# Performance work log

Measured on AMD Instinct MI355X. Metric: run time of the kernel, lower is better.

## Reference

```python
import jax, jax.numpy as jnp
import numpy as np

FEATURE_LEN = 64
DIM_ATOM = 256
DIM_GRAPH = 256
NUM_NEI = 32
B = 2048          # reactions / graphs in batch
ATOMS = 30        # atoms per molecule graph
N = B * ATOMS     # total nodes
E = 4 * N         # total edges
NMOL = 100000     # knowledge-graph molecule table size
S = 2             # molecules per reaction side (len(id_list))


def setup_inputs() -> dict:
    key = jax.random.key(0)
    ks = jax.random.split(key, 16)
    xavier = lambda k, shape: (jax.random.normal(k, shape, jnp.float32)
                               * np.sqrt(2.0 / (shape[0] + shape[-1])))
    return {
        "node_feat": jax.random.randint(ks[0], (N, 4), 0, FEATURE_LEN, jnp.int32),
        "edge_src": jax.random.randint(ks[1], (E,), 0, N, jnp.int32),
        "edge_dst": jax.random.randint(ks[2], (E,), 0, N, jnp.int32),
        "graph_ids": jnp.repeat(jnp.arange(B, dtype=jnp.int32), ATOMS),
        "id_list": jax.random.randint(ks[3], (S, B), 0, NMOL, jnp.int32),
        "id_list_target": jax.random.randint(ks[4], (S, B), 0, NMOL, jnp.int32),
        "all_mfea": (jax.random.uniform(ks[5], (NMOL, 40)) < 0.3).astype(jnp.float32),
        "neighbor_matrix": jax.random.randint(ks[6], (NMOL, NUM_NEI), 0, NMOL, jnp.int32),
        "W0": xavier(ks[7], (FEATURE_LEN, DIM_ATOM)),
        "b0": jnp.zeros((DIM_ATOM,), jnp.float32),
        "W1": xavier(ks[8], (DIM_ATOM, DIM_ATOM)),
        "b1": jnp.zeros((DIM_ATOM,), jnp.float32),
        "fea_emb": xavier(ks[9], (40, DIM_GRAPH)),
        "att_w": xavier(ks[10], (DIM_GRAPH, 1)),
        "att_b": jnp.zeros((1,), jnp.float32),
        "crosscl_w": xavier(ks[11], (DIM_GRAPH, DIM_ATOM)),
        "crosscl_b": jnp.zeros((DIM_ATOM,), jnp.float32),
    }


def reference(node_feat, edge_src, edge_dst, graph_ids, id_list, id_list_target,
              all_mfea, neighbor_matrix,
              W0, b0, W1, b1, fea_emb, att_w, att_b, crosscl_w, crosscl_b):
    n = node_feat.shape[0]
    # --- atom-level GCN (DGL GraphConv, norm='both') ---
    h = jax.nn.one_hot(node_feat, FEATURE_LEN, dtype=jnp.float32).sum(axis=1)  # [N, F]
    ones_e = jnp.ones((edge_src.shape[0],), jnp.float32)
    deg_out = jnp.clip(jax.ops.segment_sum(ones_e, edge_src, n), 1.0)
    deg_in = jnp.clip(jax.ops.segment_sum(ones_e, edge_dst, n), 1.0)
    norm_src = deg_out[:, None] ** -0.5
    norm_dst = deg_in[:, None] ** -0.5

    def gcn(x, W, b, act):
        m = (x * norm_src)[edge_src]                        # gather along edges
        agg = jax.ops.segment_sum(m, edge_dst, n)           # scatter-add
        z = (agg * norm_dst) @ W + b
        return act(z)

    h = gcn(h, W0, b0, jax.nn.relu)
    h = gcn(h, W1, b1, lambda z: z)
    # factor computed via python float() in torch -> detached constant
    factor = np.sqrt(DIM_ATOM).astype(np.float32) / jax.lax.stop_gradient(
        jnp.mean(jnp.linalg.norm(h, axis=1)))
    h = h * factor
    mol_atom_embedding = jax.ops.segment_sum(h, graph_ids, B)  # SumPooling [B, D]

    # --- reaction-level KG aggregation ---
    src_emb = jnp.einsum('sbf,fg->sbg', all_mfea[id_list], fea_emb)         # [S,B,G]
    tgt_emb = jnp.einsum('sbf,fg->sbg', all_mfea[id_list_target], fea_emb)  # [S,B,G]
    source_re = src_emb.mean(axis=0)   # 1/len * sum
    target_re = tgt_emb.mean(axis=0)

    item_emb = src_emb                                       # [S,B,G]
    nei_idx = neighbor_matrix[id_list]                       # [S,B,K]
    nei_emb = jnp.einsum('sbkf,fg->sbkg', all_mfea[nei_idx], fea_emb)  # [S,B,K,G]

    target_embedding = source_re + target_re                 # [B,G]
    score_nei = item_emb[:, :, None, :] * nei_emb * target_embedding[None, :, None, :]
    logits = score_nei @ att_w + att_b                       # [S,B,K,1]
    score_att = jax.nn.softmax(logits, axis=2)
    nei_agg = jnp.sum(score_att * nei_emb, axis=2)           # [S,B,G]

    mol_reaction_embedding = (item_emb + nei_agg).mean(axis=0)  # [B,G]
    mol_x_embedding = mol_reaction_embedding @ crosscl_w + crosscl_b
    mol_embedding = jnp.concatenate([mol_atom_embedding, mol_reaction_embedding], axis=1)
    return mol_embedding, mol_atom_embedding, mol_x_embedding
```

## Files before the change

### kernel.cpp

```cpp
#include <hip/hip_runtime.h>
#include <math.h>

#define N_NODES 61440
#define N_EDGES 245760
#define BATCH   2048
#define ATOMS   30
#define F_LEN   64
#define DIM     256
#define NUM_NEI 32
#define MF      40
#define ECAP    512
#define CH      32
#define NBG     (N_NODES / 32)

typedef __attribute__((ext_vector_type(8))) short s8v;
typedef __attribute__((ext_vector_type(4))) float f4v;
typedef __attribute__((address_space(3))) unsigned lds_u32;
typedef const __attribute__((address_space(1))) unsigned glb_u32;

__device__ __forceinline__ unsigned short f2bf(float x) {
    union { float f; unsigned u; } c; c.f = x;
    unsigned r = (c.u + 0x7FFFu + ((c.u >> 16) & 1u)) >> 16;
    return (unsigned short)r;
}
__device__ __forceinline__ float bf2f(unsigned short u) {
    union { unsigned u; float f; } c; c.u = ((unsigned)u) << 16;
    return c.f;
}
__device__ __forceinline__ float u2f(unsigned u) {
    union { unsigned u; float f; } c; c.u = u;
    return c.f;
}

__global__ __launch_bounds__(256) void k_deg_prepw(
    const int* __restrict__ esrc, const int* __restrict__ edst,
    int* deg_out, int* deg_in,
    const float* __restrict__ W0, const float* __restrict__ W1,
    unsigned short* __restrict__ w0bt, unsigned short* __restrict__ w1bt) {
    __shared__ float tile[64][65];
    int bi = blockIdx.x;
    int t = threadIdx.x;
    if (bi < 960) {
        int e = bi * 256 + t;
        atomicAdd(&deg_out[esrc[e]], 1);
        atomicAdd(&deg_in[edst[e]], 1);
        return;
    }
    int b2 = bi - 960;
    int c = t & 63, rq = t >> 6;
    if (b2 < 16) {
        int tr = b2 >> 2, tc = b2 & 3;
#pragma unroll 4
        for (int pass = 0; pass < 16; pass++) {
            int r = rq + 4 * pass;
            tile[r][c] = W1[(size_t)(tr * 64 + r) * 256 + tc * 64 + c];
        }
        __syncthreads();
#pragma unroll 4
        for (int pass = 0; pass < 16; pass++) {
            int nr = rq + 4 * pass;
            w1bt[(size_t)(tc * 64 + nr) * 256 + tr * 64 + c] = f2bf(tile[c][nr]);
        }
    } else {
        int tb = b2 - 16;
#pragma unroll 4
        for (int pass = 0; pass < 16; pass++) {
            int r = rq + 4 * pass;
            tile[r][c] = W0[(size_t)r * 256 + tb * 64 + c];
        }
        __syncthreads();
#pragma unroll 4
        for (int pass = 0; pass < 16; pass++) {
            int nr = rq + 4 * pass;
            w0bt[(size_t)(tb * 64 + nr) * 64 + c] = f2bf(tile[c][nr]);
        }
    }
}

__global__ void k_alloc(const int* __restrict__ deg_in, int* row_start, int* cursor,
                        int* counter) {
    int t = threadIdx.x;
    int n = blockIdx.x * 256 + t;
    int lane = t & 63;
    int d = deg_in[n];
    int p = d;
#pragma unroll
    for (int o = 1; o < 64; o <<= 1) { int v = __shfl_up(p, o, 64); if (lane >= o) p += v; }
    int base = 0;
    if (lane == 63) base = atomicAdd(counter, p);
    base = __shfl(base, 63, 64);
    int v = base + p - d;
    row_start[n] = v;
    cursor[n] = v;
}

__global__ void k_csr_fill(const int* __restrict__ esrc, const int* __restrict__ edst,
                           int* cursor, int* csr_src) {
    int e = blockIdx.x * 256 + threadIdx.x;
    if (e < N_EDGES) {
        int p = atomicAdd(&cursor[edst[e]], 1);
        csr_src[p] = esrc[e];
    }
}

__global__ __launch_bounds__(256) void k_gcn0(
    const int* __restrict__ nf, const int* __restrict__ row_start,
    const int* __restrict__ csr_src, const int* __restrict__ deg_in,
    const int* __restrict__ deg_out, const unsigned short* __restrict__ w0bt,
    const float* __restrict__ b0, unsigned short* __restrict__ h1b) {
    __shared__ float la0[32 * 68];
    __shared__ int4  enf[ECAP];
    __shared__ float ens[ECAP];
    __shared__ int   rs[33];
    __shared__ float lnd[32], lns[32];
    __shared__ float b0c[256];
    int n0 = blockIdx.x * 32;
    int t = threadIdx.x;
    if (t < 32) rs[t] = row_start[n0 + t];
    if (t == 0) rs[32] = row_start[n0 + 31] + deg_in[n0 + 31];
    if (t < 32) {
        lnd[t] = rsqrtf((float)max(deg_in[n0 + t], 1));
        lns[t] = rsqrtf((float)max(deg_out[n0 + t], 1));
    }
    b0c[t] = b0[t];
    for (int i = t; i < 32 * 68; i += 256) la0[i] = 0.f;
    __syncthreads();
    int beg0 = rs[0];
    int tot = rs[32] - beg0; if (tot > ECAP) tot = ECAP;
    for (int e = t; e < tot; e += 256) {
        int s = csr_src[beg0 + e];
        enf[e] = ((const int4*)nf)[s];
        ens[e] = rsqrtf((float)max(deg_out[s], 1));
    }
    __syncthreads();
    if (t < 128) {
        int row = t >> 2, fi = t & 3;
        int lo = rs[row] - beg0, hi = rs[row + 1] - beg0;
        if (hi > tot) hi = tot;
        for (int e = lo; e < hi; e++) {
            int4 f = enf[e];
            int fv = (fi == 0) ? f.x : (fi == 1) ? f.y : (fi == 2) ? f.z : f.w;
            atomicAdd(&la0[row * 68 + fv], ens[e]);
        }
    }
    __syncthreads();
    int lane = t & 63, wv = t >> 6;
    int ln = lane & 15, lg = lane >> 4;
    f4v acc[2][4];
#pragma unroll
    for (int mi = 0; mi < 2; mi++)
#pragma unroll
        for (int ni = 0; ni < 4; ni++) acc[mi][ni] = (f4v)0.f;
#pragma unroll
    for (int kst = 0; kst < 2; kst++) {
        s8v afr[2];
#pragma unroll
        for (int mi = 0; mi < 2; mi++) {
            const float* p = &la0[(mi * 16 + ln) * 68 + kst * 32 + lg * 8];
            f4v lo = *(const f4v*)p;
            f4v hi = *(const f4v*)(p + 4);
            s8v a;
#pragma unroll
            for (int j = 0; j < 4; j++) { a[j] = (short)f2bf(lo[j]); a[4 + j] = (short)f2bf(hi[j]); }
            afr[mi] = a;
        }
#pragma unroll
        for (int ni = 0; ni < 4; ni++) {
            int n = wv * 64 + ni * 16 + ln;
            s8v b = *(const s8v*)&w0bt[(size_t)n * 64 + kst * 32 + lg * 8];
            acc[0][ni] = __builtin_amdgcn_mfma_f32_16x16x32_bf16(afr[0], b, acc[0][ni], 0, 0, 0);
            acc[1][ni] = __builtin_amdgcn_mfma_f32_16x16x32_bf16(afr[1], b, acc[1][ni], 0, 0, 0);
        }
    }
#pragma unroll
    for (int mi = 0; mi < 2; mi++)
#pragma unroll
        for (int ni = 0; ni < 4; ni++) {
            int n = wv * 64 + ni * 16 + ln;
            float bb = b0c[n];
#pragma unroll
            for (int r = 0; r < 4; r++) {
                int m = mi * 16 + lg * 4 + r;
                float z = acc[mi][ni][r] * lnd[m] + bb;
                z = fmaxf(z, 0.f) * lns[m];
                h1b[(size_t)(n0 + m) * 256 + n] = f2bf(z);
            }
        }
}

__global__ __launch_bounds__(256, 4) void k_gcn1rxn(
    const unsigned short* __restrict__ h1b, const int* __restrict__ row_start,
    const int* __restrict__ csr_src, const int* __restrict__ deg_in,
    const unsigned short* __restrict__ w1bt, const float* __restrict__ b1,
    unsigned short* __restrict__ h2b, float* __restrict__ partial,
    const int* __restrict__ id_list, const int* __restrict__ id_list_t,
    const int* __restrict__ neimat, const float* __restrict__ mfea,
    const float* __restrict__ fea_emb, const float* __restrict__ att_w,
    const float* __restrict__ att_b, float* __restrict__ mre_out,
    float* __restrict__ out) {
    __shared__ __attribute__((aligned(16))) char smem[36992];
    int bid = blockIdx.x;
    int t = threadIdx.x;
    int lane = t & 63, wv = t >> 6;
    bool isg; int sub;
    if (bid < 2 * NBG) { isg = !(bid & 1); sub = bid >> 1; }
    else { isg = false; sub = NBG + (bid - 2 * NBG); }

    if (isg) {
        unsigned short* stage = (unsigned short*)smem;
        int*   ecache = (int*)(smem + 32768);
        int*   rs     = (int*)(smem + 34816);
        float* lnd    = (float*)(smem + 34960);
        float* b1c    = (float*)(smem + 35088);
        float* nsq    = (float*)(smem + 36112);
        unsigned short* lab = stage;
        int n0 = sub * 32;
        if (t < 32) rs[t] = row_start[n0 + t];
        if (t == 0) rs[32] = row_start[n0 + 31] + deg_in[n0 + 31];
        if (t < 32) {
            lnd[t] = rsqrtf((float)max(deg_in[n0 + t], 1));
            nsq[t] = 0.f;
        }
        b1c[t] = b1[t];
        __syncthreads();
        int beg0 = rs[0];
        int tot = rs[32] - beg0; if (tot > ECAP) tot = ECAP;
        for (int e = t; e < tot; e += 256) ecache[e] = csr_src[beg0 + e];
        __syncthreads();

        int gr = t >> 5;
        int gc = (t & 31) * 8;
        int lo[4], hi[4];
#pragma unroll
        for (int r = 0; r < 4; r++) {
            int i = gr + r * 8;
            lo[r] = rs[i] - beg0;
            int h = rs[i + 1] - beg0; if (h > tot) h = tot;
            hi[r] = h;
        }
        float a[4][8];
#pragma unroll
        for (int r = 0; r < 4; r++)
#pragma unroll
            for (int j = 0; j < 8; j++) a[r][j] = 0.f;

        int lhalf = lane >> 5;
        int colo = (lane & 31) * 8;
        int nc = (tot + CH - 1) >> 5;
#define ISSUE(c)                                                                   \
        {                                                                          \
            int base_ = (c) << 5;                                                  \
            unsigned short* sb_ = stage + ((c) & 1) * (CH * 256);                  \
            _Pragma("unroll")                                                      \
            for (int pp = 0; pp < 4; ++pp) {                                       \
                int p_ = wv + pp * 4;                                              \
                int e_ = base_ + 2 * p_ + lhalf;                                   \
                int sv_ = ecache[min(e_, tot - 1)];                                \
                __builtin_amdgcn_global_load_lds(                                  \
                    (glb_u32*)(h1b + (size_t)sv_ * 256 + colo),                    \
                    (lds_u32*)(sb_ + 2 * p_ * 256), 16, 0, 0);                     \
            }                                                                      \
        }
        if (nc > 0) ISSUE(0);
        for (int c = 0; c < nc; ++c) {
            if (c + 1 < nc) {
                ISSUE(c + 1);
                asm volatile("s_waitcnt vmcnt(4)" ::: "memory");
            } else {
                asm volatile("s_waitcnt vmcnt(0)" ::: "memory");
            }
            __builtin_amdgcn_sched_barrier(0);
            __builtin_amdgcn_s_barrier();
            int c0 = c << 5;
            int nch = min(CH, tot - c0);
            const unsigned short* sb = stage + (c & 1) * (CH * 256);
#pragma unroll
            for (int r = 0; r < 4; r++) {
                int es = max(lo[r] - c0, 0);
                int ee = min(hi[r] - c0, nch);
                for (int e = es; e < ee; e++) {
                    s8v v = *(const s8v*)&sb[e * 256 + gc];
#pragma unroll
                    for (int j = 0; j < 8; j++) a[r][j] += bf2f((unsigned short)v[j]);
                }
            }
            __builtin_amdgcn_s_barrier();
        }
#undef ISSUE
#pragma unroll
        for (int r = 0; r < 4; r++) {
            int i = gr + r * 8;
            s8v ov;
#pragma unroll
            for (int j = 0; j < 8; j++) ov[j] = (short)f2bf(a[r][j]);
            *(s8v*)&lab[i * 264 + gc] = ov;
        }
        __syncthreads();
        int ln = lane & 15, lg = lane >> 4;
        f4v acc[2][4];
#pragma unroll
        for (int mi = 0; mi < 2; mi++)
#pragma unroll
            for (int ni = 0; ni < 4; ni++) acc[mi][ni] = (f4v)0.f;
#pragma unroll 2
        for (int kst = 0; kst < 8; kst++) {
            s8v afr[2];
#pragma unroll
            for (int mi = 0; mi < 2; mi++)
                afr[mi] = *(const s8v*)&lab[(mi * 16 + ln) * 264 + kst * 32 + lg * 8];
#pragma unroll
            for (int ni = 0; ni < 4; ni++) {
                int n = wv * 64 + ni * 16 + ln;
                s8v b = *(const s8v*)&w1bt[(size_t)n * 256 + kst * 32 + lg * 8];
                acc[0][ni] = __builtin_amdgcn_mfma_f32_16x16x32_bf16(afr[0], b, acc[0][ni], 0, 0, 0);
                acc[1][ni] = __builtin_amdgcn_mfma_f32_16x16x32_bf16(afr[1], b, acc[1][ni], 0, 0, 0);
            }
        }
        float sm[2][4];
#pragma unroll
        for (int mi = 0; mi < 2; mi++)
#pragma unroll
            for (int r = 0; r < 4; r++) sm[mi][r] = 0.f;
#pragma unroll
        for (int mi = 0; mi < 2; mi++)
#pragma unroll
            for (int ni = 0; ni < 4; ni++) {
                int n = wv * 64 + ni * 16 + ln;
                float bb = b1c[n];
#pragma unroll
                for (int r = 0; r < 4; r++) {
                    int m = mi * 16 + lg * 4 + r;
                    float z = acc[mi][ni][r] * lnd[m] + bb;
                    h2b[(size_t)(n0 + m) * 256 + n] = f2bf(z);
                    sm[mi][r] += z * z;
                }
            }
#pragma unroll
        for (int mi = 0; mi < 2; mi++)
#pragma unroll
            for (int r = 0; r < 4; r++) {
                float v = sm[mi][r];
                v += __shfl_xor(v, 1);
                v += __shfl_xor(v, 2);
                v += __shfl_xor(v, 4);
                v += __shfl_xor(v, 8);
                if (ln == 0) atomicAdd(&nsq[mi * 16 + lg * 4 + r], v);
            }
        __syncthreads();
        if (t < 32) atomicAdd(&partial[(n0 + t) & 1023], sqrtf(nsq[t]));
    } else {
        float* com   = (float*)smem;
        float* mitem = (float*)(smem + 160);
        float* u     = (float*)(smem + 320);
        float* nm    = (float*)(smem + 1344);
        float* vv    = (float*)(smem + 6464);
        float* aw    = (float*)(smem + 6624);
        int b = sub;
        if (t < MF) {
            int i0 = id_list[b], i1 = id_list[BATCH + b];
            int j0 = id_list_t[b], j1 = id_list_t[BATCH + b];
            com[t] = 0.5f * (mfea[(size_t)i0 * MF + t] + mfea[(size_t)i1 * MF + t])
                   + 0.5f * (mfea[(size_t)j0 * MF + t] + mfea[(size_t)j1 * MF + t]);
        }
        __syncthreads();
        float tg = 0.f;
        for (int f = 0; f < MF; f++) tg += com[f] * fea_emb[f * DIM + t];
        float awt = att_w[t];
        float msum = 0.f;
        for (int s = 0; s < 2; s++) {
            int id = id_list[s * BATCH + b];
            __syncthreads();
            if (t < MF) mitem[t] = mfea[(size_t)id * MF + t];
            for (int i = t; i < NUM_NEI * 10; i += 256) {
                int k = i / 10, q = i - k * 10;
                int nid = neimat[(size_t)id * NUM_NEI + k];
                *(float4*)&nm[k * MF + q * 4] = *(const float4*)&mfea[(size_t)nid * MF + q * 4];
            }
            __syncthreads();
            float item = 0.f;
            for (int f = 0; f < MF; f++) item += mitem[f] * fea_emb[f * DIM + t];
            u[t] = item * tg * awt;
            __syncthreads();
            for (int i = 0; i < 5; i++) {
                int f = wv + 8 * i;
                float p = 0.f;
#pragma unroll
                for (int j = 0; j < 4; j++) p += u[lane + 64 * j] * fea_emb[f * DIM + lane + 64 * j];
#pragma unroll
                for (int off = 32; off; off >>= 1) p += __shfl_down(p, off, 64);
                if (lane == 0) vv[f] = p;
            }
            __syncthreads();
            if (wv == 0) {
                float lg2 = -1e30f;
                if (lane < NUM_NEI) {
                    lg2 = att_b[0];
                    for (int f = 0; f < MF; f++) lg2 += nm[lane * MF + f] * vv[f];
                }
                float m = lg2;
#pragma unroll
                for (int off = 16; off; off >>= 1) m = fmaxf(m, __shfl_xor(m, off, 32));
                float e = (lane < NUM_NEI) ? __expf(lg2 - m) : 0.f;
                float ssum = e;
#pragma unroll
                for (int off = 16; off; off >>= 1) ssum += __shfl_xor(ssum, off, 32);
                if (lane < NUM_NEI) aw[lane] = e / ssum;
            }
            __syncthreads();
            if (t < MF) {
                float w = 0.f;
                for (int k = 0; k < NUM_NEI; k++) w += aw[k] * nm[k * MF + t];
                vv[t] = w;
            }
            __syncthreads();
            float na = 0.f;
            for (int f = 0; f < MF; f++) na += vv[f] * fea_emb[f * DIM + t];
            msum += item + na;
        }
        float m = 0.5f * msum;
        out[(size_t)b * 512 + DIM + t] = m;
        mre_out[(size_t)b * DIM + t] = m;
    }
}

__global__ __launch_bounds__(256) void k_fin(
    const unsigned short* __restrict__ h2b, const float* __restrict__ partial,
    const float* __restrict__ mre, const float* __restrict__ cw,
    const float* __restrict__ cb, float* __restrict__ out) {
    __shared__ float red[256];
    __shared__ float lm[8 * DIM];
    int t = threadIdx.x;
    int b0 = blockIdx.x * 8;
    float s = partial[t] + partial[t + 256] + partial[t + 512] + partial[t + 768];
    red[t] = s;
    __syncthreads();
    for (int o = 128; o; o >>= 1) {
        if (t < o) red[t] += red[t + o];
        __syncthreads();
    }
    float fac = 16.0f * (float)N_NODES / red[0];
#pragma unroll 2
    for (int i = 0; i < 8; i++) {
        float pv = 0.f;
        for (int a = 0; a < ATOMS; a++)
            pv += bf2f(h2b[(size_t)((b0 + i) * ATOMS + a) * DIM + t]);
        pv *= fac;
        out[(size_t)(b0 + i) * 512 + t] = pv;
        out[(size_t)BATCH * 512 + (size_t)(b0 + i) * DIM + t] = pv;
    }
    for (int i = t; i < 8 * DIM / 4; i += 256)
        ((float4*)lm)[i] = ((const float4*)(mre + (size_t)b0 * DIM))[i];
    __syncthreads();
    float acc[8];
    float bb = cb[t];
#pragma unroll
    for (int i = 0; i < 8; i++) acc[i] = bb;
    for (int uu = 0; uu < DIM; uu++) {
        float w = cw[(size_t)uu * DIM + t];
#pragma unroll
        for (int i = 0; i < 8; i++) acc[i] += lm[i * DIM + uu] * w;
    }
#pragma unroll
    for (int i = 0; i < 8; i++)
        out[(size_t)BATCH * 768 + (size_t)(b0 + i) * DIM + t] = acc[i];
}

extern "C" void kernel_launch(void* const* d_in, const int* in_sizes, int n_in,
                              void* d_out, int out_size, void* d_ws, size_t ws_size,
                              hipStream_t stream) {
    const int*   node_feat = (const int*)d_in[0];
    const int*   edge_src  = (const int*)d_in[1];
    const int*   edge_dst  = (const int*)d_in[2];
    const int*   id_list   = (const int*)d_in[4];
    const int*   id_list_t = (const int*)d_in[5];
    const float* all_mfea  = (const float*)d_in[6];
    const int*   neimat    = (const int*)d_in[7];
    const float* W0        = (const float*)d_in[8];
    const float* b0        = (const float*)d_in[9];
    const float* W1        = (const float*)d_in[10];
    const float* b1        = (const float*)d_in[11];
    const float* fea_emb   = (const float*)d_in[12];
    const float* att_w     = (const float*)d_in[13];
    const float* att_b     = (const float*)d_in[14];
    const float* crosscl_w = (const float*)d_in[15];
    const float* crosscl_b = (const float*)d_in[16];
    float* out = (float*)d_out;

    char* ws = (char*)d_ws;
    char* zbase = ws;
    int*   deg_out   = (int*)ws;            ws += (size_t)N_NODES * 4;
    int*   deg_in    = (int*)ws;            ws += (size_t)N_NODES * 4;
    float* partial   = (float*)ws;          ws += 1024 * 4;
    int*   counter   = (int*)(ws + 8);      ws += 256;
    size_t zbytes = (size_t)(ws - zbase);
    int*   row_start = (int*)ws;            ws += (size_t)N_NODES * 4;
    int*   cursor    = (int*)ws;            ws += (size_t)N_NODES * 4;
    int*   csr_srcb  = (int*)ws;            ws += (size_t)N_EDGES * 4;
    unsigned short* w0bt = (unsigned short*)ws; ws += (size_t)256 * 64 * 2;
    unsigned short* w1bt = (unsigned short*)ws; ws += (size_t)256 * 256 * 2;
    unsigned short* h1b  = (unsigned short*)ws; ws += (size_t)N_NODES * DIM * 2;
    unsigned short* h2b  = (unsigned short*)ws; ws += (size_t)N_NODES * DIM * 2;
    float* mre       = (float*)ws;          ws += (size_t)BATCH * DIM * 4;

    hipMemsetAsync(zbase, 0, zbytes, stream);

    k_deg_prepw<<<980, 256, 0, stream>>>(edge_src, edge_dst, deg_out, deg_in,
                                         W0, W1, w0bt, w1bt);
    k_alloc<<<N_NODES / 256, 256, 0, stream>>>(deg_in, row_start, cursor, counter);
    k_csr_fill<<<(N_EDGES + 255) / 256, 256, 0, stream>>>(edge_src, edge_dst, cursor, csr_srcb);
    k_gcn0<<<N_NODES / 32, 256, 0, stream>>>(node_feat, row_start, csr_srcb, deg_in,
                                             deg_out, w0bt, b0, h1b);
    k_gcn1rxn<<<2 * NBG + (BATCH - NBG), 256, 0, stream>>>(
        h1b, row_start, csr_srcb, deg_in, w1bt, b1, h2b, partial,
        id_list, id_list_t, neimat, all_mfea, fea_emb, att_w, att_b, mre, out);
    k_fin<<<BATCH / 8, 256, 0, stream>>>(h2b, partial, mre, crosscl_w, crosscl_b, out);
}
```

Measured before the change: 198.2 us.

## Split fused GCN-layer-1 and reaction kernel into two separate launches

Splits the combined kernel, which interleaved GCN layer-1 aggregation/GEMM blocks with reaction-level KG attention blocks, into two kernels launched back to back on the same stream. Each kernel now has its own static shared-memory footprint, so the light reaction kernel no longer reserves the large staging buffer and may reach higher occupancy. The cost is an extra launch and the loss of overlap between the memory-bound gather work and the latency-bound reaction work.

Result: faster. 186.1 us (median of 3 runs) (-6.1%).

```diff
diff --git a/kernel.cpp b/kernel.cpp
--- a/kernel.cpp
+++ b/kernel.cpp
@@ -11,7 +11,6 @@
 #define MF      40
 #define ECAP    512
 #define CH      32
-#define NBG     (N_NODES / 32)
 
 typedef __attribute__((ext_vector_type(8))) short s8v;
 typedef __attribute__((ext_vector_type(4))) float f4v;
@@ -25,10 +24,6 @@
 }
 __device__ __forceinline__ float bf2f(unsigned short u) {
     union { unsigned u; float f; } c; c.u = ((unsigned)u) << 16;
-    return c.f;
-}
-__device__ __forceinline__ float u2f(unsigned u) {
-    union { unsigned u; float f; } c; c.u = u;
     return c.f;
 }
 
@@ -188,239 +183,235 @@
         }
 }
 
-__global__ __launch_bounds__(256, 4) void k_gcn1rxn(
+__global__ __launch_bounds__(256, 4) void k_gcn1(
     const unsigned short* __restrict__ h1b, const int* __restrict__ row_start,
     const int* __restrict__ csr_src, const int* __restrict__ deg_in,
     const unsigned short* __restrict__ w1bt, const float* __restrict__ b1,
-    unsigned short* __restrict__ h2b, float* __restrict__ partial,
+    unsigned short* __restrict__ h2b, float* __restrict__ partial) {
+    __shared__ unsigned short stage[2 * CH * 256];
+    __shared__ int   ecache[ECAP];
+    __shared__ int   rs[33];
+    __shared__ float lnd[32];
+    __shared__ float b1c[256];
+    __shared__ float nsq[32];
+    unsigned short* lab = stage;
+    int n0 = blockIdx.x * 32;
+    int t = threadIdx.x;
+    int lane = t & 63, wv = t >> 6;
+    if (t < 32) rs[t] = row_start[n0 + t];
+    if (t == 0) rs[32] = row_start[n0 + 31] + deg_in[n0 + 31];
+    if (t < 32) {
+        lnd[t] = rsqrtf((float)max(deg_in[n0 + t], 1));
+        nsq[t] = 0.f;
+    }
+    b1c[t] = b1[t];
+    __syncthreads();
+    int beg0 = rs[0];
+    int tot = rs[32] - beg0; if (tot > ECAP) tot = ECAP;
+    for (int e = t; e < tot; e += 256) ecache[e] = csr_src[beg0 + e];
+    __syncthreads();
+
+    int gr = t >> 5;
+    int gc = (t & 31) * 8;
+    int lo[4], hi[4];
+#pragma unroll
+    for (int r = 0; r < 4; r++) {
+        int i = gr + r * 8;
+        lo[r] = rs[i] - beg0;
+        int h = rs[i + 1] - beg0; if (h > tot) h = tot;
+        hi[r] = h;
+    }
+    float a[4][8];
+#pragma unroll
+    for (int r = 0; r < 4; r++)
+#pragma unroll
+        for (int j = 0; j < 8; j++) a[r][j] = 0.f;
+
+    int lhalf = lane >> 5;
+    int colo = (lane & 31) * 8;
+    int nc = (tot + CH - 1) >> 5;
+#define ISSUE(c)                                                                   \
+    {                                                                              \
+        int base_ = (c) << 5;                                                      \
+        unsigned short* sb_ = stage + ((c) & 1) * (CH * 256);                      \
+        _Pragma("unroll")                                                          \
+        for (int pp = 0; pp < 4; ++pp) {                                           \
+            int p_ = wv + pp * 4;                                                  \
+            int e_ = base_ + 2 * p_ + lhalf;                                       \
+            int sv_ = ecache[min(e_, tot - 1)];                                    \
+            __builtin_amdgcn_global_load_lds(                                      \
+                (glb_u32*)(h1b + (size_t)sv_ * 256 + colo),                        \
+                (lds_u32*)(sb_ + 2 * p_ * 256), 16, 0, 0);                         \
+        }                                                                          \
+    }
+    if (nc > 0) ISSUE(0);
+    for (int c = 0; c < nc; ++c) {
+        if (c + 1 < nc) {
+            ISSUE(c + 1);
+            asm volatile("s_waitcnt vmcnt(4)" ::: "memory");
+        } else {
+            asm volatile("s_waitcnt vmcnt(0)" ::: "memory");
+        }
+        __builtin_amdgcn_sched_barrier(0);
+        __builtin_amdgcn_s_barrier();
+        int c0 = c << 5;
+        int nch = min(CH, tot - c0);
+        const unsigned short* sb = stage + (c & 1) * (CH * 256);
+#pragma unroll
+        for (int r = 0; r < 4; r++) {
+            int es = max(lo[r] - c0, 0);
+            int ee = min(hi[r] - c0, nch);
+            for (int e = es; e < ee; e++) {
+                s8v v = *(const s8v*)&sb[e * 256 + gc];
+#pragma unroll
+                for (int j = 0; j < 8; j++) a[r][j] += bf2f((unsigned short)v[j]);
+            }
+        }
+        __builtin_amdgcn_s_barrier();
+    }
+#undef ISSUE
+#pragma unroll
+    for (int r = 0; r < 4; r++) {
+        int i = gr + r * 8;
+        s8v ov;
+#pragma unroll
+        for (int j = 0; j < 8; j++) ov[j] = (short)f2bf(a[r][j]);
+        *(s8v*)&lab[i * 264 + gc] = ov;
+    }
+    __syncthreads();
+    int ln = lane & 15, lg = lane >> 4;
+    f4v acc[2][4];
+#pragma unroll
+    for (int mi = 0; mi < 2; mi++)
+#pragma unroll
+        for (int ni = 0; ni < 4; ni++) acc[mi][ni] = (f4v)0.f;
+#pragma unroll 2
+    for (int kst = 0; kst < 8; kst++) {
+        s8v afr[2];
+#pragma unroll
+        for (int mi = 0; mi < 2; mi++)
+            afr[mi] = *(const s8v*)&lab[(mi * 16 + ln) * 264 + kst * 32 + lg * 8];
+#pragma unroll
+        for (int ni = 0; ni < 4; ni++) {
+            int n = wv * 64 + ni * 16 + ln;
+            s8v b = *(const s8v*)&w1bt[(size_t)n * 256 + kst * 32 + lg * 8];
+            acc[0][ni] = __builtin_amdgcn_mfma_f32_16x16x32_bf16(afr[0], b, acc[0][ni], 0, 0, 0);
+            acc[1][ni] = __builtin_amdgcn_mfma_f32_16x16x32_bf16(afr[1], b, acc[1][ni], 0, 0, 0);
+        }
+    }
+    float sm[2][4];
+#pragma unroll
+    for (int mi = 0; mi < 2; mi++)
+#pragma unroll
+        for (int r = 0; r < 4; r++) sm[mi][r] = 0.f;
+#pragma unroll
+    for (int mi = 0; mi < 2; mi++)
+#pragma unroll
+        for (int ni = 0; ni < 4; ni++) {
+            int n = wv * 64 + ni * 16 + ln;
+            float bb = b1c[n];
+#pragma unroll
+            for (int r = 0; r < 4; r++) {
+                int m = mi * 16 + lg * 4 + r;
+                float z = acc[mi][ni][r] * lnd[m] + bb;
+                h2b[(size_t)(n0 + m) * 256 + n] = f2bf(z);
+                sm[mi][r] += z * z;
+            }
+        }
+#pragma unroll
+    for (int mi = 0; mi < 2; mi++)
+#pragma unroll
+        for (int r = 0; r < 4; r++) {
+            float v = sm[mi][r];
+            v += __shfl_xor(v, 1);
+            v += __shfl_xor(v, 2);
+            v += __shfl_xor(v, 4);
+            v += __shfl_xor(v, 8);
+            if (ln == 0) atomicAdd(&nsq[mi * 16 + lg * 4 + r], v);
+        }
+    __syncthreads();
+    if (t < 32) atomicAdd(&partial[(n0 + t) & 1023], sqrtf(nsq[t]));
+}
+
+__global__ __launch_bounds__(256) void k_rxn(
     const int* __restrict__ id_list, const int* __restrict__ id_list_t,
     const int* __restrict__ neimat, const float* __restrict__ mfea,
     const float* __restrict__ fea_emb, const float* __restrict__ att_w,
     const float* __restrict__ att_b, float* __restrict__ mre_out,
     float* __restrict__ out) {
-    __shared__ __attribute__((aligned(16))) char smem[36992];
-    int bid = blockIdx.x;
+    __shared__ float com[MF];
+    __shared__ float mitem[MF];
+    __shared__ float u[DIM];
+    __shared__ float nm[NUM_NEI * MF];
+    __shared__ float vv[MF];
+    __shared__ float aw[NUM_NEI];
+    int b = blockIdx.x;
     int t = threadIdx.x;
-    int lane = t & 63, wv = t >> 6;
-    bool isg; int sub;
-    if (bid < 2 * NBG) { isg = !(bid & 1); sub = bid >> 1; }
-    else { isg = false; sub = NBG + (bid - 2 * NBG); }
-
-    if (isg) {
-        unsigned short* stage = (unsigned short*)smem;
-        int*   ecache = (int*)(smem + 32768);
-        int*   rs     = (int*)(smem + 34816);
-        float* lnd    = (float*)(smem + 34960);
-        float* b1c    = (float*)(smem + 35088);
-        float* nsq    = (float*)(smem + 36112);
-        unsigned short* lab = stage;
-        int n0 = sub * 32;
-        if (t < 32) rs[t] = row_start[n0 + t];
-        if (t == 0) rs[32] = row_start[n0 + 31] + deg_in[n0 + 31];
-        if (t < 32) {
-            lnd[t] = rsqrtf((float)max(deg_in[n0 + t], 1));
-            nsq[t] = 0.f;
-        }
-        b1c[t] = b1[t];
-        __syncthreads();
-        int beg0 = rs[0];
-        int tot = rs[32] - beg0; if (tot > ECAP) tot = ECAP;
-        for (int e = t; e < tot; e += 256) ecache[e] = csr_src[beg0 + e];
-        __syncthreads();
-
-        int gr = t >> 5;
-        int gc = (t & 31) * 8;
-        int lo[4], hi[4];
-#pragma unroll
-        for (int r = 0; r < 4; r++) {
-            int i = gr + r * 8;
-            lo[r] = rs[i] - beg0;
-            int h = rs[i + 1] - beg0; if (h > tot) h = tot;
-            hi[r] = h;
-        }
-        float a[4][8];
-#pragma unroll
-        for (int r = 0; r < 4; r++)
-#pragma unroll
-            for (int j = 0; j < 8; j++) a[r][j] = 0.f;
-
-        int lhalf = lane >> 5;
-        int colo = (lane & 31) * 8;
-        int nc = (tot + CH - 1) >> 5;
-#define ISSUE(c)                                                                   \
-        {                                                                          \
-            int base_ = (c) << 5;                                                  \
-            unsigned short* sb_ = stage + ((c) & 1) * (CH * 256);                  \
-            _Pragma("unroll")                                                      \
-            for (int pp = 0; pp < 4; ++pp) {                                       \
-                int p_ = wv + pp * 4;                                              \
-                int e_ = base_ + 2 * p_ + lhalf;                                   \
-                int sv_ = ecache[min(e_, tot - 1)];                                \
-                __builtin_amdgcn_global_load_lds(                                  \
-                    (glb_u32*)(h1b + (size_t)sv_ * 256 + colo),                    \
-                    (lds_u32*)(sb_ + 2 * p_ * 256), 16, 0, 0);                     \
-            }                                                                      \
-        }
-        if (nc > 0) ISSUE(0);
-        for (int c = 0; c < nc; ++c) {
-            if (c + 1 < nc) {
-                ISSUE(c + 1);
-                asm volatile("s_waitcnt vmcnt(4)" ::: "memory");
-            } else {
-                asm volatile("s_waitcnt vmcnt(0)" ::: "memory");
+    int wv = t >> 6, lane = t & 63;
+    if (t < MF) {
+        int i0 = id_list[b], i1 = id_list[BATCH + b];
+        int j0 = id_list_t[b], j1 = id_list_t[BATCH + b];
+        com[t] = 0.5f * (mfea[(size_t)i0 * MF + t] + mfea[(size_t)i1 * MF + t])
+               + 0.5f * (mfea[(size_t)j0 * MF + t] + mfea[(size_t)j1 * MF + t]);
+    }
+    __syncthreads();
+    float tg = 0.f;
+    for (int f = 0; f < MF; f++) tg += com[f] * fea_emb[f * DIM + t];
+    float awt = att_w[t];
+    float msum = 0.f;
+    for (int s = 0; s < 2; s++) {
+        int id = id_list[s * BATCH + b];
+        __syncthreads();
+        if (t < MF) mitem[t] = mfea[(size_t)id * MF + t];
+        for (int i = t; i < NUM_NEI * 10; i += 256) {
+            int k = i / 10, q = i - k * 10;
+            int nid = neimat[(size_t)id * NUM_NEI + k];
+            *(float4*)&nm[k * MF + q * 4] = *(const float4*)&mfea[(size_t)nid * MF + q * 4];
+        }
+        __syncthreads();
+        float item = 0.f;
+        for (int f = 0; f < MF; f++) item += mitem[f] * fea_emb[f * DIM + t];
+        u[t] = item * tg * awt;
+        __syncthreads();
+        for (int i = 0; i < 5; i++) {
+            int f = wv + 8 * i;
+            float p = 0.f;
+#pragma unroll
+            for (int j = 0; j < 4; j++) p += u[lane + 64 * j] * fea_emb[f * DIM + lane + 64 * j];
+#pragma unroll
+            for (int off = 32; off; off >>= 1) p += __shfl_down(p, off, 64);
+            if (lane == 0) vv[f] = p;
+        }
+        __syncthreads();
+        if (wv == 0) {
+            float lg2 = -1e30f;
+            if (lane < NUM_NEI) {
+                lg2 = att_b[0];
+                for (int f = 0; f < MF; f++) lg2 += nm[lane * MF + f] * vv[f];
             }
-            __builtin_amdgcn_sched_barrier(0);
-            __builtin_amdgcn_s_barrier();
-            int c0 = c << 5;
-            int nch = min(CH, tot - c0);
-            const unsigned short* sb = stage + (c & 1) * (CH * 256);
-#pragma unroll
-            for (int r = 0; r < 4; r++) {
-                int es = max(lo[r] - c0, 0);
-                int ee = min(hi[r] - c0, nch);
-                for (int e = es; e < ee; e++) {
-                    s8v v = *(const s8v*)&sb[e * 256 + gc];
-#pragma unroll
-                    for (int j = 0; j < 8; j++) a[r][j] += bf2f((unsigned short)v[j]);
-                }
-            }
-            __builtin_amdgcn_s_barrier();
-        }
-#undef ISSUE
-#pragma unroll
-        for (int r = 0; r < 4; r++) {
-            int i = gr + r * 8;
-            s8v ov;
-#pragma unroll
-            for (int j = 0; j < 8; j++) ov[j] = (short)f2bf(a[r][j]);
-            *(s8v*)&lab[i * 264 + gc] = ov;
-        }
-        __syncthreads();
-        int ln = lane & 15, lg = lane >> 4;
-        f4v acc[2][4];
-#pragma unroll
-        for (int mi = 0; mi < 2; mi++)
-#pragma unroll
-            for (int ni = 0; ni < 4; ni++) acc[mi][ni] = (f4v)0.f;
-#pragma unroll 2
-        for (int kst = 0; kst < 8; kst++) {
-            s8v afr[2];
-#pragma unroll
-            for (int mi = 0; mi < 2; mi++)
-                afr[mi] = *(const s8v*)&lab[(mi * 16 + ln) * 264 + kst * 32 + lg * 8];
-#pragma unroll
-            for (int ni = 0; ni < 4; ni++) {
-                int n = wv * 64 + ni * 16 + ln;
-                s8v b = *(const s8v*)&w1bt[(size_t)n * 256 + kst * 32 + lg * 8];
-                acc[0][ni] = __builtin_amdgcn_mfma_f32_16x16x32_bf16(afr[0], b, acc[0][ni], 0, 0, 0);
-                acc[1][ni] = __builtin_amdgcn_mfma_f32_16x16x32_bf16(afr[1], b, acc[1][ni], 0, 0, 0);
-            }
-        }
-        float sm[2][4];
-#pragma unroll
-        for (int mi = 0; mi < 2; mi++)
-#pragma unroll
-            for (int r = 0; r < 4; r++) sm[mi][r] = 0.f;
-#pragma unroll
-        for (int mi = 0; mi < 2; mi++)
-#pragma unroll
-            for (int ni = 0; ni < 4; ni++) {
-                int n = wv * 64 + ni * 16 + ln;
-                float bb = b1c[n];
-#pragma unroll
-                for (int r = 0; r < 4; r++) {
-                    int m = mi * 16 + lg * 4 + r;
-                    float z = acc[mi][ni][r] * lnd[m] + bb;
-                    h2b[(size_t)(n0 + m) * 256 + n] = f2bf(z);
-                    sm[mi][r] += z * z;
-                }
-            }
-#pragma unroll
-        for (int mi = 0; mi < 2; mi++)
-#pragma unroll
-            for (int r = 0; r < 4; r++) {
-                float v = sm[mi][r];
-                v += __shfl_xor(v, 1);
-                v += __shfl_xor(v, 2);
-                v += __shfl_xor(v, 4);
-                v += __shfl_xor(v, 8);
-                if (ln == 0) atomicAdd(&nsq[mi * 16 + lg * 4 + r], v);
-            }
-        __syncthreads();
-        if (t < 32) atomicAdd(&partial[(n0 + t) & 1023], sqrtf(nsq[t]));
-    } else {
-        float* com   = (float*)smem;
-        float* mitem = (float*)(smem + 160);
-        float* u     = (float*)(smem + 320);
-        float* nm    = (float*)(smem + 1344);
-        float* vv    = (float*)(smem + 6464);
-        float* aw    = (float*)(smem + 6624);
-        int b = sub;
+            float m = lg2;
+#pragma unroll
+            for (int off = 16; off; off >>= 1) m = fmaxf(m, __shfl_xor(m, off, 32));
+            float e = (lane < NUM_NEI) ? __expf(lg2 - m) : 0.f;
+            float ssum = e;
+#pragma unroll
+            for (int off = 16; off; off >>= 1) ssum += __shfl_xor(ssum, off, 32);
+            if (lane < NUM_NEI) aw[lane] = e / ssum;
+        }
+        __syncthreads();
         if (t < MF) {
-            int i0 = id_list[b], i1 = id_list[BATCH + b];
-            int j0 = id_list_t[b], j1 = id_list_t[BATCH + b];
-            com[t] = 0.5f * (mfea[(size_t)i0 * MF + t] + mfea[(size_t)i1 * MF + t])
-                   + 0.5f * (mfea[(size_t)j0 * MF + t] + mfea[(size_t)j1 * MF + t]);
-        }
-        __syncthreads();
-        float tg = 0.f;
-        for (int f = 0; f < MF; f++) tg += com[f] * fea_emb[f * DIM + t];
-        float awt = att_w[t];
-        float msum = 0.f;
-        for (int s = 0; s < 2; s++) {
-            int id = id_list[s * BATCH + b];
-            __syncthreads();
-            if (t < MF) mitem[t] = mfea[(size_t)id * MF + t];
-            for (int i = t; i < NUM_NEI * 10; i += 256) {
-                int k = i / 10, q = i - k * 10;
-                int nid = neimat[(size_t)id * NUM_NEI + k];
-                *(float4*)&nm[k * MF + q * 4] = *(const float4*)&mfea[(size_t)nid * MF + q * 4];
-            }
-            __syncthreads();
-            float item = 0.f;
-            for (int f = 0; f < MF; f++) item += mitem[f] * fea_emb[f * DIM + t];
-            u[t] = item * tg * awt;
-            __syncthreads();
-            for (int i = 0; i < 5; i++) {
-                int f = wv + 8 * i;
-                float p = 0.f;
-#pragma unroll
-                for (int j = 0; j < 4; j++) p += u[lane + 64 * j] * fea_emb[f * DIM + lane + 64 * j];
-#pragma unroll
-                for (int off = 32; off; off >>= 1) p += __shfl_down(p, off, 64);
-                if (lane == 0) vv[f] = p;
-            }
-            __syncthreads();
-            if (wv == 0) {
-                float lg2 = -1e30f;
-                if (lane < NUM_NEI) {
-                    lg2 = att_b[0];
-                    for (int f = 0; f < MF; f++) lg2 += nm[lane * MF + f] * vv[f];
-                }
-                float m = lg2;
-#pragma unroll
-                for (int off = 16; off; off >>= 1) m = fmaxf(m, __shfl_xor(m, off, 32));
-                float e = (lane < NUM_NEI) ? __expf(lg2 - m) : 0.f;
-                float ssum = e;
-#pragma unroll
-                for (int off = 16; off; off >>= 1) ssum += __shfl_xor(ssum, off, 32);
-                if (lane < NUM_NEI) aw[lane] = e / ssum;
-            }
-            __syncthreads();
-            if (t < MF) {
-                float w = 0.f;
-                for (int k = 0; k < NUM_NEI; k++) w += aw[k] * nm[k * MF + t];
-                vv[t] = w;
-            }
-            __syncthreads();
-            float na = 0.f;
-            for (int f = 0; f < MF; f++) na += vv[f] * fea_emb[f * DIM + t];
-            msum += item + na;
-        }
-        float m = 0.5f * msum;
-        out[(size_t)b * 512 + DIM + t] = m;
-        mre_out[(size_t)b * DIM + t] = m;
-    }
+            float w = 0.f;
+            for (int k = 0; k < NUM_NEI; k++) w += aw[k] * nm[k * MF + t];
+            vv[t] = w;
+        }
+        __syncthreads();
+        float na = 0.f;
+        for (int f = 0; f < MF; f++) na += vv[f] * fea_emb[f * DIM + t];
+        msum += item + na;
+    }
+    float m = 0.5f * msum;
+    out[(size_t)b * 512 + DIM + t] = m;
+    mre_out[(size_t)b * DIM + t] = m;
 }
 
 __global__ __launch_bounds__(256) void k_fin(
@@ -510,8 +501,9 @@
     k_csr_fill<<<(N_EDGES + 255) / 256, 256, 0, stream>>>(edge_src, edge_dst, cursor, csr_srcb);
     k_gcn0<<<N_NODES / 32, 256, 0, stream>>>(node_feat, row_start, csr_srcb, deg_in,
                                              deg_out, w0bt, b0, h1b);
-    k_gcn1rxn<<<2 * NBG + (BATCH - NBG), 256, 0, stream>>>(
-        h1b, row_start, csr_srcb, deg_in, w1bt, b1, h2b, partial,
-        id_list, id_list_t, neimat, all_mfea, fea_emb, att_w, att_b, mre, out);
+    k_gcn1<<<N_NODES / 32, 256, 0, stream>>>(h1b, row_start, csr_srcb, deg_in,
+                                             w1bt, b1, h2b, partial);
+    k_rxn<<<BATCH, 256, 0, stream>>>(id_list, id_list_t, neimat, all_mfea, fea_emb,
+                                     att_w, att_b, mre, out);
     k_fin<<<BATCH / 8, 256, 0, stream>>>(h2b, partial, mre, crosscl_w, crosscl_b, out);
 }
```
